# Performance work log

Measured on AMD Instinct MI355X. Metric: run time of the kernel, lower is better.

## Reference

```python
import jax, jax.numpy as jnp
import numpy as np

B, S, H, OUT, L = 32, 4096, 128, 128, 3


def _log_g(x):
    return jnp.where(x >= 0, jnp.log(jax.nn.relu(x) + 0.5), -jax.nn.softplus(-x))


def _cell(x, Wz, bz, Wh, bh):
    # x: [B, S, Din] -> h: [B, S, H]
    k = x @ Wz.T + bz                              # [B,S,H]
    log_z = -jax.nn.softplus(-k)
    log_coeffs = -jax.nn.softplus(k)
    # h_0 = zeros -> log_g(0) = log(0.5)
    log_h0 = jnp.full((x.shape[0], 1, k.shape[-1]), np.log(0.5), dtype=k.dtype)
    log_tilde_h = _log_g(x @ Wh.T + bh)
    log_values = jnp.concatenate([log_h0, log_z + log_tilde_h], axis=1)  # [B,S+1,H]
    # FAITHFUL to source: cumsum over the FEATURE axis (dim=-1), pad along seq
    a_star = jnp.pad(jnp.cumsum(log_coeffs, axis=-1), ((0, 0), (1, 0), (0, 0)))
    log_h = a_star + jax.lax.cumlogsumexp(log_values - a_star, axis=1)
    # torch forward applies sigmoid to the cell output, then drops the h_0 row
    return jax.nn.sigmoid(jnp.exp(log_h))[:, 1:, :]


def setup_inputs() -> dict:
    key = jax.random.key(0)
    ks = jax.random.split(key, 2 * L + 2)
    inp = {"x": jax.random.normal(ks[0], (B, S), dtype=jnp.float32)}
    for l in range(L):
        din = 1 if l == 0 else H
        inp[f"Wz{l}"] = jax.random.normal(ks[1 + 2 * l], (H, din), dtype=jnp.float32) * 0.02
        inp[f"bz{l}"] = jnp.zeros((H,), dtype=jnp.float32)
        inp[f"Wh{l}"] = jax.random.normal(ks[2 + 2 * l], (H, din), dtype=jnp.float32) * 0.02
        inp[f"bh{l}"] = jnp.zeros((H,), dtype=jnp.float32)
    inp["Wout"] = jax.random.normal(ks[-1], (OUT, H * S), dtype=jnp.float32) * (1.0 / np.sqrt(H * S))
    inp["bout"] = jnp.zeros((OUT,), dtype=jnp.float32)
    return inp


def reference(x, Wz0, bz0, Wh0, bh0, Wz1, bz1, Wh1, bh1, Wz2, bz2, Wh2, bh2, Wout, bout):
    h = x[:, :, None]  # [B,S,1]
    for (Wz, bz, Wh, bh) in ((Wz0, bz0, Wh0, bh0), (Wz1, bz1, Wh1, bh1), (Wz2, bz2, Wh2, bh2)):
        h = _cell(h, Wz, bz, Wh, bh)
    flat = h.reshape(h.shape[0], -1)  # [B, S*H]
    return flat @ Wout.T + bout       # [B, OUT]
```

## Files before the change

### kernel.cpp

```cpp
#include <hip/hip_runtime.h>
#include <hip/hip_bf16.h>
#include <math.h>

#define B_   32
#define S_   4096
#define H_   128
#define OUT_ 128
#define P_   (B_*S_)
#define NC_  64
#define CH_  (S_/NC_)
#define NKS_ 512
#define KTOT_ (H_*S_)
#define NEGINF_ (-__builtin_inff())
#define HTP_ 136

typedef __bf16 bf16x8 __attribute__((ext_vector_type(8)));
typedef float  f32x4  __attribute__((ext_vector_type(4)));
typedef unsigned short ushort8_t __attribute__((ext_vector_type(8)));

__device__ __forceinline__ float l1p_(float x) { return __logf(1.f + x); }

__device__ __forceinline__ float sp_(float x) {
  return fmaxf(x, 0.f) + l1p_(__expf(-fabsf(x)));
}
__device__ __forceinline__ float logg_(float x) {
  return (x >= 0.f) ? __logf(x + 0.5f) : -sp_(-x);
}
__device__ __forceinline__ float lae_(float a, float b) {
  float m = fmaxf(a, b);
  float d = fminf(a, b) - m;
  return m + l1p_(__expf(d));
}
__device__ __forceinline__ float sigm_(float e) {
  return __builtin_amdgcn_rcpf(1.f + __expf(-e));
}
__device__ __forceinline__ unsigned short f2bf_(float f) {
  unsigned int u = __float_as_uint(f);
  u += 0x7fffu + ((u >> 16) & 1u);
  return (unsigned short)(u >> 16);
}
__device__ __forceinline__ float wscan_(float v) {
  int lane = threadIdx.x & 63;
  #pragma unroll
  for (int d = 1; d < 64; d <<= 1) {
    float t = __shfl_up(v, (unsigned)d, 64);
    if (lane >= d) v += t;
  }
  return v;
}

__global__ __launch_bounds__(256) void convw2_kernel(
    const float* __restrict__ Wz1, const float* __restrict__ Wh1,
    const float* __restrict__ Wz2, const float* __restrict__ Wh2,
    unsigned short* __restrict__ Wc1, unsigned short* __restrict__ Wc2)
{
  int idx = blockIdx.x * 256 + threadIdx.x;
  Wc1[idx] = f2bf_(idx < 16384 ? Wz1[idx] : Wh1[idx - 16384]);
  Wc2[idx] = f2bf_(idx < 16384 ? Wz2[idx] : Wh2[idx - 16384]);
}

__global__ __launch_bounds__(128) void prep0t_kernel(
    const float* __restrict__ x,
    const float* __restrict__ Wz, const float* __restrict__ bz,
    const float* __restrict__ Wh, const float* __restrict__ bh,
    float* __restrict__ u, float* __restrict__ A, float* __restrict__ tot)
{
  __shared__ float tl[128];
  int lane = threadIdx.x & 63, wid = threadIdx.x >> 6;
  float wz0 = Wz[lane], wz1 = Wz[lane + 64];
  float bz0 = bz[lane], bz1 = bz[lane + 64];
  float wh0 = Wh[lane], wh1 = Wh[lane + 64];
  float bh0 = bh[lane], bh1 = bh[lane + 64];
  int blk = blockIdx.x;
  size_t base = (size_t)blk * (CH_ * H_);
  int pos0 = blk * CH_;
  float t0 = NEGINF_, t1 = NEGINF_;
  for (int j = 0; j < 32; ++j) {
    int i = j * 2 + wid;
    float xv = x[pos0 + i];
    float k0 = fmaf(xv, wz0, bz0), k1 = fmaf(xv, wz1, bz1);
    float g0 = fmaf(xv, wh0, bh0), g1 = fmaf(xv, wh1, bh1);
    float lc0 = -sp_(k0), lc1 = -sp_(k1);
    float lv0 = k0 + lc0 + logg_(g0);
    float lv1 = k1 + lc1 + logg_(g1);
    float s0 = wscan_(lc0);
    float c0 = __shfl(s0, 63, 64);
    float s1 = wscan_(lc1) + c0;
    float u0 = lv0 - s0, u1 = lv1 - s1;
    size_t o = base + (size_t)i * H_;
    u[o + lane]      = u0;  u[o + 64 + lane] = u1;
    A[o + lane]      = s0;  A[o + 64 + lane] = s1;
    t0 = lae_(t0, u0); t1 = lae_(t1, u1);
  }
  if (wid == 0) { tl[lane] = t0; tl[64 + lane] = t1; }
  __syncthreads();
  if (wid == 1) {
    tot[(size_t)blk * H_ + lane]      = lae_(tl[lane], t0);
    tot[(size_t)blk * H_ + 64 + lane] = lae_(tl[64 + lane], t1);
  }
}

__global__ __launch_bounds__(128) void scan2_kernel(
    const float* __restrict__ tot, float* __restrict__ carry)
{
  int b = blockIdx.x, ch = threadIdx.x;
  float r = -0.6931471805599453f;
  for (int c = 0; c < NC_; ++c) {
    size_t idx = (size_t)(b * NC_ + c) * H_ + ch;
    carry[idx] = r;
    r = lae_(r, tot[idx]);
  }
}

__global__ __launch_bounds__(128) void kb_kernel(
    const float* __restrict__ carry,
    const unsigned short* __restrict__ Wc,
    const float* __restrict__ bz, const float* __restrict__ bh,
    float* __restrict__ u, float* __restrict__ A,
    float* __restrict__ tot)
{
  __shared__ unsigned short hT[64][HTP_];
  __shared__ float kg[16][260];
  __shared__ float tl[128];
  int tid = threadIdx.x;
  int lane = tid & 63, w = tid >> 6;
  int l15 = lane & 15, quad = lane >> 4;
  int blk = blockIdx.x;
  size_t base = (size_t)blk * (CH_ * H_);

  {
    int ch = tid;
    float r = carry[(size_t)blk * H_ + ch];
    const float* up = u + base + ch;
    const float* Ap = A + base + ch;
    for (int i0 = 0; i0 < CH_; i0 += 16) {
      float uv[16], av[16];
      #pragma unroll
      for (int i = 0; i < 16; ++i) { uv[i] = up[(i0 + i) * H_]; av[i] = Ap[(i0 + i) * H_]; }
      #pragma unroll
      for (int i = 0; i < 16; ++i) {
        r = lae_(r, uv[i]);
        float hv = sigm_(__expf(av[i] + r));
        hT[i0 + i][ch] = f2bf_(hv);
      }
    }
  }
  __syncthreads();

  float bz0v = bz[lane], bz1v = bz[lane + 64];
  float bh0v = bh[lane], bh1v = bh[lane + 64];
  float t0 = NEGINF_, t1 = NEGINF_;

  for (int t = 0; t < 4; ++t) {
    f32x4 z = {0.f, 0.f, 0.f, 0.f};
    f32x4 acc[8] = {z, z, z, z, z, z, z, z};
    #pragma unroll
    for (int kk = 0; kk < 4; ++kk) {
      bf16x8 a = *reinterpret_cast<const bf16x8*>(&hT[t * 16 + l15][kk * 32 + quad * 8]);
      #pragma unroll
      for (int nt = 0; nt < 8; ++nt) {
        int n = w * 128 + nt * 16 + l15;
        bf16x8 bf = *reinterpret_cast<const bf16x8*>(Wc + n * 128 + kk * 32 + quad * 8);
        acc[nt] = __builtin_amdgcn_mfma_f32_16x16x32_bf16(a, bf, acc[nt], 0, 0, 0);
      }
    }
    __syncthreads();
    #pragma unroll
    for (int nt = 0; nt < 8; ++nt) {
      int col = w * 128 + nt * 16 + l15;
      #pragma unroll
      for (int r2 = 0; r2 < 4; ++r2)
        kg[quad * 4 + r2][col] = acc[nt][r2];
    }
    __syncthreads();
    #pragma unroll
    for (int i = 0; i < 8; ++i) {
      int row = w + i * 2;
      int sIdx = t * 16 + row;
      float k0 = kg[row][lane]        + bz0v;
      float k1 = kg[row][64 + lane]   + bz1v;
      float g0 = kg[row][128 + lane]  + bh0v;
      float g1 = kg[row][192 + lane]  + bh1v;
      float lc0 = -sp_(k0), lc1 = -sp_(k1);
      float lv0 = k0 + lc0 + logg_(g0);
      float lv1 = k1 + lc1 + logg_(g1);
      float s0 = wscan_(lc0);
      float c0 = __shfl(s0, 63, 64);
      float s1 = wscan_(lc1) + c0;
      float u0 = lv0 - s0, u1 = lv1 - s1;
      size_t o = base + (size_t)sIdx * H_;
      u[o + lane]      = u0;  u[o + 64 + lane] = u1;
      A[o + lane]      = s0;  A[o + 64 + lane] = s1;
      t0 = lae_(t0, u0); t1 = lae_(t1, u1);
    }
  }

  __syncthreads();
  if (w == 0) { tl[lane] = t0; tl[64 + lane] = t1; }
  __syncthreads();
  if (w == 1) {
    tot[(size_t)blk * H_ + lane]      = lae_(tl[lane], t0);
    tot[(size_t)blk * H_ + 64 + lane] = lae_(tl[64 + lane], t1);
  }
}

__global__ __launch_bounds__(128) void scan3v2_kernel(
    const float* __restrict__ u, const float* __restrict__ A,
    const float* __restrict__ carry, unsigned short* __restrict__ hbf)
{
  int blk = blockIdx.x, ch = threadIdx.x;
  size_t base = (size_t)blk * (CH_ * H_);
  float r = carry[(size_t)blk * H_ + ch];
  const float* up = u + base + ch;
  const float* Ap = A + base + ch;
  unsigned short* hp = hbf + base + ch;
  for (int i0 = 0; i0 < CH_; i0 += 16) {
    float uv[16], av[16];
    #pragma unroll
    for (int i = 0; i < 16; ++i) { uv[i] = up[(i0 + i) * H_]; av[i] = Ap[(i0 + i) * H_]; }
    #pragma unroll
    for (int i = 0; i < 16; ++i) {
      r = lae_(r, uv[i]);
      float hv = sigm_(__expf(av[i] + r));
      hp[(size_t)(i0 + i) * H_] = f2bf_(hv);
    }
  }
}

__global__ __launch_bounds__(256) void outmm_kernel(
    const unsigned short* __restrict__ hbf,
    const float* __restrict__ Wout,
    float* __restrict__ part)
{
  const int KSL = KTOT_ / NKS_;
  int tid = threadIdx.x, w = tid >> 6, lane = tid & 63;
  int l15 = lane & 15, quad = lane >> 4;
  int k0base = blockIdx.x * KSL;
  f32x4 acc[2][2] = {{{0,0,0,0},{0,0,0,0}},{{0,0,0,0},{0,0,0,0}}};
  for (int ks = 0; ks < KSL; ks += 32) {
    int k0 = k0base + ks;
    bf16x8 a0 = *reinterpret_cast<const bf16x8*>(
        hbf + (size_t)l15 * KTOT_ + k0 + quad * 8);
    bf16x8 a1 = *reinterpret_cast<const bf16x8*>(
        hbf + (size_t)(16 + l15) * KTOT_ + k0 + quad * 8);
    #pragma unroll
    for (int nt = 0; nt < 2; ++nt) {
      int n = w * 32 + nt * 16 + l15;
      const float* wp = Wout + (size_t)n * KTOT_ + k0 + quad * 8;
      float4 wa = *reinterpret_cast<const float4*>(wp);
      float4 wb = *reinterpret_cast<const float4*>(wp + 4);
      ushort8_t tt;
      tt[0] = f2bf_(wa.x); tt[1] = f2bf_(wa.y); tt[2] = f2bf_(wa.z); tt[3] = f2bf_(wa.w);
      tt[4] = f2bf_(wb.x); tt[5] = f2bf_(wb.y); tt[6] = f2bf_(wb.z); tt[7] = f2bf_(wb.w);
      bf16x8 bf = __builtin_bit_cast(bf16x8, tt);
      acc[0][nt] = __builtin_amdgcn_mfma_f32_16x16x32_bf16(a0, bf, acc[0][nt], 0, 0, 0);
      acc[1][nt] = __builtin_amdgcn_mfma_f32_16x16x32_bf16(a1, bf, acc[1][nt], 0, 0, 0);
    }
  }
  float* pp = part + (size_t)blockIdx.x * (B_ * OUT_);
  #pragma unroll
  for (int mt = 0; mt < 2; ++mt)
    #pragma unroll
    for (int nt = 0; nt < 2; ++nt)
      #pragma unroll
      for (int r = 0; r < 4; ++r) {
        int b = mt * 16 + quad * 4 + r;
        int o = w * 32 + nt * 16 + l15;
        pp[b * OUT_ + o] = acc[mt][nt][r];
      }
}

__global__ __launch_bounds__(256) void outred_kernel(
    const float* __restrict__ part, const float* __restrict__ bout,
    float* __restrict__ out)
{
  int w = threadIdx.x >> 6, lane = threadIdx.x & 63;
  int idx = blockIdx.x * 4 + w;
  float s = 0.f;
  for (int wg = lane; wg < NKS_; wg += 64) s += part[(size_t)wg * (B_ * OUT_) + idx];
  #pragma unroll
  for (int d = 32; d; d >>= 1) s += __shfl_down(s, (unsigned)d, 64);
  if (lane == 0) out[idx] = s + bout[idx & (OUT_ - 1)];
}

extern "C" void kernel_launch(void* const* d_in, const int* in_sizes, int n_in,
                              void* d_out, int out_size, void* d_ws, size_t ws_size,
                              hipStream_t stream)
{
  const float* x    = (const float*)d_in[0];
  const float* Wz[3] = {(const float*)d_in[1], (const float*)d_in[5], (const float*)d_in[9]};
  const float* bz[3] = {(const float*)d_in[2], (const float*)d_in[6], (const float*)d_in[10]};
  const float* Wh[3] = {(const float*)d_in[3], (const float*)d_in[7], (const float*)d_in[11]};
  const float* bh[3] = {(const float*)d_in[4], (const float*)d_in[8], (const float*)d_in[12]};
  const float* Wout = (const float*)d_in[13];
  const float* bout = (const float*)d_in[14];
  float* out = (float*)d_out;

  char* ws = (char*)d_ws;
  float*          u     = (float*)(ws + 0);
  float*          A     = (float*)(ws + 67108864);
  unsigned short* hbf   = (unsigned short*)(ws + 134217728);
  unsigned short* Wc1   = (unsigned short*)(ws + 167772160);
  unsigned short* Wc2   = (unsigned short*)(ws + 167837696);
  float*          tot   = (float*)(ws + 167903232);
  float*          carry = (float*)(ws + 168951808);
  float*          part  = (float*)(ws + 170000384);

  convw2_kernel<<<128, 256, 0, stream>>>(Wz[1], Wh[1], Wz[2], Wh[2], Wc1, Wc2);

  prep0t_kernel<<<B_ * NC_, 128, 0, stream>>>(x, Wz[0], bz[0], Wh[0], bh[0], u, A, tot);
  scan2_kernel<<<B_, 128, 0, stream>>>(tot, carry);

  kb_kernel<<<B_ * NC_, 128, 0, stream>>>(carry, Wc1, bz[1], bh[1], u, A, tot);
  scan2_kernel<<<B_, 128, 0, stream>>>(tot, carry);
  kb_kernel<<<B_ * NC_, 128, 0, stream>>>(carry, Wc2, bz[2], bh[2], u, A, tot);
  scan2_kernel<<<B_, 128, 0, stream>>>(tot, carry);

  scan3v2_kernel<<<B_ * NC_, 128, 0, stream>>>(u, A, carry, hbf);

  outmm_kernel<<<NKS_, 256, 0, stream>>>(hbf, Wout, part);
  outred_kernel<<<(B_ * OUT_) / 4, 256, 0, stream>>>(part, bout, out);
}
```

Before: 743.7 us.

## Double threads per chunk, split intra-chunk scan, use DPP wave scan and cheaper math

Blocks of prep0t, kb and scan3 grow to 256 threads. The sequential 64-step log-sum-exp scan inside each chunk is split into two 32-step halves: one half runs from the carry, the other computes a local prefix that is later combined through shared memory. The MFMA tile work in kb is spread over 4 waves instead of 2. The shuffle-based wave prefix sum is replaced with DPP row-shift and row-broadcast adds, and softplus, log_g and logaddexp are rewritten with fewer transcendentals. The intent is to shorten serial dependency chains and raise occupancy. The trade-offs are larger LDS use per block and less numerically stable softplus for large inputs, which can overflow exp.

```diff
diff --git a/kernel.cpp b/kernel.cpp
--- a/kernel.cpp
+++ b/kernel.cpp
@@ -18,18 +18,17 @@
 typedef float  f32x4  __attribute__((ext_vector_type(4)));
 typedef unsigned short ushort8_t __attribute__((ext_vector_type(8)));
 
-__device__ __forceinline__ float l1p_(float x) { return __logf(1.f + x); }
-
 __device__ __forceinline__ float sp_(float x) {
-  return fmaxf(x, 0.f) + l1p_(__expf(-fabsf(x)));
+  return __logf(1.f + __expf(x));
 }
 __device__ __forceinline__ float logg_(float x) {
-  return (x >= 0.f) ? __logf(x + 0.5f) : -sp_(-x);
+  float t = (x >= 0.f) ? (x + 0.5f) : __builtin_amdgcn_rcpf(1.f + __expf(-x));
+  return __logf(t);
 }
 __device__ __forceinline__ float lae_(float a, float b) {
   float m = fmaxf(a, b);
-  float d = fminf(a, b) - m;
-  return m + l1p_(__expf(d));
+  float d = -fabsf(a - b);
+  return m + __logf(1.f + __expf(d));
 }
 __device__ __forceinline__ float sigm_(float e) {
   return __builtin_amdgcn_rcpf(1.f + __expf(-e));
@@ -39,13 +38,17 @@
   u += 0x7fffu + ((u >> 16) & 1u);
   return (unsigned short)(u >> 16);
 }
+
+#define DPPADD_(v, ctrl, rmask) \
+  ((v) + __int_as_float(__builtin_amdgcn_update_dpp( \
+      0, __float_as_int(v), (ctrl), (rmask), 0xf, true)))
 __device__ __forceinline__ float wscan_(float v) {
-  int lane = threadIdx.x & 63;
-  #pragma unroll
-  for (int d = 1; d < 64; d <<= 1) {
-    float t = __shfl_up(v, (unsigned)d, 64);
-    if (lane >= d) v += t;
-  }
+  v = DPPADD_(v, 0x111, 0xf);
+  v = DPPADD_(v, 0x112, 0xf);
+  v = DPPADD_(v, 0x114, 0xf);
+  v = DPPADD_(v, 0x118, 0xf);
+  v = DPPADD_(v, 0x142, 0xa);
+  v = DPPADD_(v, 0x143, 0xc);
   return v;
 }
 
@@ -59,14 +62,14 @@
   Wc2[idx] = f2bf_(idx < 16384 ? Wz2[idx] : Wh2[idx - 16384]);
 }
 
-__global__ __launch_bounds__(128) void prep0t_kernel(
+__global__ __launch_bounds__(256) void prep0t_kernel(
     const float* __restrict__ x,
     const float* __restrict__ Wz, const float* __restrict__ bz,
     const float* __restrict__ Wh, const float* __restrict__ bh,
     float* __restrict__ u, float* __restrict__ A, float* __restrict__ tot)
 {
-  __shared__ float tl[128];
-  int lane = threadIdx.x & 63, wid = threadIdx.x >> 6;
+  __shared__ float tpart[4][128];
+  int lane = threadIdx.x & 63, w = threadIdx.x >> 6;
   float wz0 = Wz[lane], wz1 = Wz[lane + 64];
   float bz0 = bz[lane], bz1 = bz[lane + 64];
   float wh0 = Wh[lane], wh1 = Wh[lane + 64];
@@ -75,8 +78,8 @@
   size_t base = (size_t)blk * (CH_ * H_);
   int pos0 = blk * CH_;
   float t0 = NEGINF_, t1 = NEGINF_;
-  for (int j = 0; j < 32; ++j) {
-    int i = j * 2 + wid;
+  for (int j = 0; j < 16; ++j) {
+    int i = j * 4 + w;
     float xv = x[pos0 + i];
     float k0 = fmaf(xv, wz0, bz0), k1 = fmaf(xv, wz1, bz1);
     float g0 = fmaf(xv, wh0, bh0), g1 = fmaf(xv, wh1, bh1);
@@ -92,11 +95,15 @@
     A[o + lane]      = s0;  A[o + 64 + lane] = s1;
     t0 = lae_(t0, u0); t1 = lae_(t1, u1);
   }
-  if (wid == 0) { tl[lane] = t0; tl[64 + lane] = t1; }
-  __syncthreads();
-  if (wid == 1) {
-    tot[(size_t)blk * H_ + lane]      = lae_(tl[lane], t0);
-    tot[(size_t)blk * H_ + 64 + lane] = lae_(tl[64 + lane], t1);
+  tpart[w][lane] = t0; tpart[w][64 + lane] = t1;
+  __syncthreads();
+  if (w == 0) {
+    int ch = lane;
+    tot[(size_t)blk * H_ + ch] =
+        lae_(lae_(tpart[0][ch], tpart[1][ch]), lae_(tpart[2][ch], tpart[3][ch]));
+    ch = lane + 64;
+    tot[(size_t)blk * H_ + ch] =
+        lae_(lae_(tpart[0][ch], tpart[1][ch]), lae_(tpart[2][ch], tpart[3][ch]));
   }
 }
 
@@ -112,7 +119,7 @@
   }
 }
 
-__global__ __launch_bounds__(128) void kb_kernel(
+__global__ __launch_bounds__(256) void kb_kernel(
     const float* __restrict__ carry,
     const unsigned short* __restrict__ Wc,
     const float* __restrict__ bz, const float* __restrict__ bh,
@@ -121,27 +128,54 @@
 {
   __shared__ unsigned short hT[64][HTP_];
   __shared__ float kg[16][260];
-  __shared__ float tl[128];
+  __shared__ float scr[32][128];
+  __shared__ float thand[128];
+  __shared__ float tpart[4][128];
   int tid = threadIdx.x;
   int lane = tid & 63, w = tid >> 6;
   int l15 = lane & 15, quad = lane >> 4;
+  int half = tid >> 7, ch = tid & 127;
   int blk = blockIdx.x;
   size_t base = (size_t)blk * (CH_ * H_);
 
-  {
-    int ch = tid;
+  if (half == 0) {
     float r = carry[(size_t)blk * H_ + ch];
     const float* up = u + base + ch;
     const float* Ap = A + base + ch;
-    for (int i0 = 0; i0 < CH_; i0 += 16) {
+    for (int i0 = 0; i0 < 32; i0 += 16) {
       float uv[16], av[16];
       #pragma unroll
       for (int i = 0; i < 16; ++i) { uv[i] = up[(i0 + i) * H_]; av[i] = Ap[(i0 + i) * H_]; }
       #pragma unroll
       for (int i = 0; i < 16; ++i) {
         r = lae_(r, uv[i]);
-        float hv = sigm_(__expf(av[i] + r));
-        hT[i0 + i][ch] = f2bf_(hv);
+        hT[i0 + i][ch] = f2bf_(sigm_(__expf(av[i] + r)));
+      }
+    }
+    thand[ch] = r;
+  } else {
+    float r = NEGINF_;
+    const float* up = u + base + ch;
+    for (int i0 = 0; i0 < 32; i0 += 16) {
+      float uv[16];
+      #pragma unroll
+      for (int i = 0; i < 16; ++i) uv[i] = up[(32 + i0 + i) * H_];
+      #pragma unroll
+      for (int i = 0; i < 16; ++i) { r = lae_(r, uv[i]); scr[i0 + i][ch] = r; }
+    }
+  }
+  __syncthreads();
+  if (half == 1) {
+    float r31 = thand[ch];
+    const float* Ap = A + base + ch;
+    for (int i0 = 0; i0 < 32; i0 += 16) {
+      float av[16];
+      #pragma unroll
+      for (int i = 0; i < 16; ++i) av[i] = Ap[(32 + i0 + i) * H_];
+      #pragma unroll
+      for (int i = 0; i < 16; ++i) {
+        float ri = lae_(r31, scr[i0 + i][ch]);
+        hT[32 + i0 + i][ch] = f2bf_(sigm_(__expf(av[i] + ri)));
       }
     }
   }
@@ -153,29 +187,29 @@
 
   for (int t = 0; t < 4; ++t) {
     f32x4 z = {0.f, 0.f, 0.f, 0.f};
-    f32x4 acc[8] = {z, z, z, z, z, z, z, z};
+    f32x4 acc[4] = {z, z, z, z};
     #pragma unroll
     for (int kk = 0; kk < 4; ++kk) {
       bf16x8 a = *reinterpret_cast<const bf16x8*>(&hT[t * 16 + l15][kk * 32 + quad * 8]);
       #pragma unroll
-      for (int nt = 0; nt < 8; ++nt) {
-        int n = w * 128 + nt * 16 + l15;
+      for (int nt = 0; nt < 4; ++nt) {
+        int n = w * 64 + nt * 16 + l15;
         bf16x8 bf = *reinterpret_cast<const bf16x8*>(Wc + n * 128 + kk * 32 + quad * 8);
         acc[nt] = __builtin_amdgcn_mfma_f32_16x16x32_bf16(a, bf, acc[nt], 0, 0, 0);
       }
     }
     __syncthreads();
     #pragma unroll
-    for (int nt = 0; nt < 8; ++nt) {
-      int col = w * 128 + nt * 16 + l15;
+    for (int nt = 0; nt < 4; ++nt) {
+      int col = w * 64 + nt * 16 + l15;
       #pragma unroll
       for (int r2 = 0; r2 < 4; ++r2)
         kg[quad * 4 + r2][col] = acc[nt][r2];
     }
     __syncthreads();
     #pragma unroll
-    for (int i = 0; i < 8; ++i) {
-      int row = w + i * 2;
+    for (int i = 0; i < 4; ++i) {
+      int row = w + i * 4;
       int sIdx = t * 16 + row;
       float k0 = kg[row][lane]        + bz0v;
       float k1 = kg[row][64 + lane]   + bz1v;
@@ -195,34 +229,66 @@
     }
   }
 
-  __syncthreads();
-  if (w == 0) { tl[lane] = t0; tl[64 + lane] = t1; }
-  __syncthreads();
-  if (w == 1) {
-    tot[(size_t)blk * H_ + lane]      = lae_(tl[lane], t0);
-    tot[(size_t)blk * H_ + 64 + lane] = lae_(tl[64 + lane], t1);
-  }
-}
-
-__global__ __launch_bounds__(128) void scan3v2_kernel(
+  tpart[w][lane] = t0; tpart[w][64 + lane] = t1;
+  __syncthreads();
+  if (w == 0) {
+    int c = lane;
+    tot[(size_t)blk * H_ + c] =
+        lae_(lae_(tpart[0][c], tpart[1][c]), lae_(tpart[2][c], tpart[3][c]));
+    c = lane + 64;
+    tot[(size_t)blk * H_ + c] =
+        lae_(lae_(tpart[0][c], tpart[1][c]), lae_(tpart[2][c], tpart[3][c]));
+  }
+}
+
+__global__ __launch_bounds__(256) void scan3v2_kernel(
     const float* __restrict__ u, const float* __restrict__ A,
     const float* __restrict__ carry, unsigned short* __restrict__ hbf)
 {
-  int blk = blockIdx.x, ch = threadIdx.x;
+  __shared__ float scr[32][128];
+  __shared__ float thand[128];
+  int tid = threadIdx.x;
+  int half = tid >> 7, ch = tid & 127;
+  int blk = blockIdx.x;
   size_t base = (size_t)blk * (CH_ * H_);
-  float r = carry[(size_t)blk * H_ + ch];
   const float* up = u + base + ch;
   const float* Ap = A + base + ch;
   unsigned short* hp = hbf + base + ch;
-  for (int i0 = 0; i0 < CH_; i0 += 16) {
-    float uv[16], av[16];
-    #pragma unroll
-    for (int i = 0; i < 16; ++i) { uv[i] = up[(i0 + i) * H_]; av[i] = Ap[(i0 + i) * H_]; }
-    #pragma unroll
-    for (int i = 0; i < 16; ++i) {
-      r = lae_(r, uv[i]);
-      float hv = sigm_(__expf(av[i] + r));
-      hp[(size_t)(i0 + i) * H_] = f2bf_(hv);
+  if (half == 0) {
+    float r = carry[(size_t)blk * H_ + ch];
+    for (int i0 = 0; i0 < 32; i0 += 16) {
+      float uv[16], av[16];
+      #pragma unroll
+      for (int i = 0; i < 16; ++i) { uv[i] = up[(i0 + i) * H_]; av[i] = Ap[(i0 + i) * H_]; }
+      #pragma unroll
+      for (int i = 0; i < 16; ++i) {
+        r = lae_(r, uv[i]);
+        hp[(size_t)(i0 + i) * H_] = f2bf_(sigm_(__expf(av[i] + r)));
+      }
+    }
+    thand[ch] = r;
+  } else {
+    float r = NEGINF_;
+    for (int i0 = 0; i0 < 32; i0 += 16) {
+      float uv[16];
+      #pragma unroll
+      for (int i = 0; i < 16; ++i) uv[i] = up[(32 + i0 + i) * H_];
+      #pragma unroll
+      for (int i = 0; i < 16; ++i) { r = lae_(r, uv[i]); scr[i0 + i][ch] = r; }
+    }
+  }
+  __syncthreads();
+  if (half == 1) {
+    float r31 = thand[ch];
+    for (int i0 = 0; i0 < 32; i0 += 16) {
+      float av[16];
+      #pragma unroll
+      for (int i = 0; i < 16; ++i) av[i] = Ap[(32 + i0 + i) * H_];
+      #pragma unroll
+      for (int i = 0; i < 16; ++i) {
+        float ri = lae_(r31, scr[i0 + i][ch]);
+        hp[(size_t)(32 + i0 + i) * H_] = f2bf_(sigm_(__expf(av[i] + ri)));
+      }
     }
   }
 }
@@ -308,15 +374,15 @@
 
   convw2_kernel<<<128, 256, 0, stream>>>(Wz[1], Wh[1], Wz[2], Wh[2], Wc1, Wc2);
 
-  prep0t_kernel<<<B_ * NC_, 128, 0, stream>>>(x, Wz[0], bz[0], Wh[0], bh[0], u, A, tot);
+  prep0t_kernel<<<B_ * NC_, 256, 0, stream>>>(x, Wz[0], bz[0], Wh[0], bh[0], u, A, tot);
   scan2_kernel<<<B_, 128, 0, stream>>>(tot, carry);
 
-  kb_kernel<<<B_ * NC_, 128, 0, stream>>>(carry, Wc1, bz[1], bh[1], u, A, tot);
+  kb_kernel<<<B_ * NC_, 256, 0, stream>>>(carry, Wc1, bz[1], bh[1], u, A, tot);
   scan2_kernel<<<B_, 128, 0, stream>>>(tot, carry);
-  kb_kernel<<<B_ * NC_, 128, 0, stream>>>(carry, Wc2, bz[2], bh[2], u, A, tot);
+  kb_kernel<<<B_ * NC_, 256, 0, stream>>>(carry, Wc2, bz[2], bh[2], u, A, tot);
   scan2_kernel<<<B_, 128, 0, stream>>>(tot, carry);
 
-  scan3v2_kernel<<<B_ * NC_, 128, 0, stream>>>(u, A, carry, hbf);
+  scan3v2_kernel<<<B_ * NC_, 256, 0, stream>>>(u, A, carry, hbf);
 
   outmm_kernel<<<NKS_, 256, 0, stream>>>(hbf, Wout, part);
   outred_kernel<<<(B_ * OUT_) / 4, 256, 0, stream>>>(part, bout, out);
```

Result: faster. 667.0 us (-10.3%).
